# Performance work log

Measured on AMD Instinct MI355X. Metric: run time of the kernel, lower is better.

The kernel has to match this reference:

```python
import jax, jax.numpy as jnp
import numpy as np

D_MODEL = 1024
NUM_HEADS = 16
BATCH = 2
SEQ = 2048


def setup_inputs() -> dict:
    key = jax.random.key(0)
    ks = jax.random.split(key, 5)
    scale = 1.0 / np.sqrt(D_MODEL)
    x = jax.random.normal(ks[0], (BATCH, SEQ, D_MODEL), dtype=jnp.float32)
    Wq = jax.random.normal(ks[1], (D_MODEL, D_MODEL), dtype=jnp.float32) * scale
    Wk = jax.random.normal(ks[2], (D_MODEL, D_MODEL), dtype=jnp.float32) * scale
    Wv = jax.random.normal(ks[3], (D_MODEL, D_MODEL), dtype=jnp.float32) * scale
    Wo = jax.random.normal(ks[4], (D_MODEL, D_MODEL), dtype=jnp.float32) * scale
    return {"x": x, "Wq": Wq, "Wk": Wk, "Wv": Wv, "Wo": Wo}


def reference(x, Wq, Wk, Wv, Wo):
    b, s, d_model = x.shape
    h = NUM_HEADS
    d_head = d_model // h
    # projections (Linear with weight [out,in]: y = x @ W^T)
    def split_heads(y):
        return y.reshape(b, s, h, d_head).transpose(0, 2, 1, 3)  # b h s d
    q = split_heads(x @ Wq.T)
    k = split_heads(x @ Wk.T)
    v = split_heads(x @ Wv.T)
    # full (non-flash) attention, as in the original
    att = jnp.einsum('bhsd,bhtd->bhst', q, k) / jnp.sqrt(jnp.float32(d_head)).astype(x.dtype)
    att = jax.nn.softmax(att, axis=-1)
    out = jnp.einsum('bhst,bhtd->bhsd', att, v)
    out = out.transpose(0, 2, 1, 3).reshape(b, s, d_model)
    return out @ Wo.T
```

## Files before the change

### kernel.cpp

```cpp
#include <hip/hip_runtime.h>
#include <stdint.h>

typedef __bf16 bf16_t;
typedef __bf16 bf16x4 __attribute__((ext_vector_type(4)));
typedef __bf16 bf16x8 __attribute__((ext_vector_type(8)));
typedef float  f32x4  __attribute__((ext_vector_type(4)));

#define D_MODEL 1024
#define SEQ     2048
#define BATCH   2
#define NHEAD   16
#define DHEAD   64
#define NROWS   (BATCH*SEQ)
#define LDK     40
#define LDT     68

__device__ __forceinline__ int sig64(int i) { return ((i & 3) << 4) | (i >> 2); }

__device__ __forceinline__ bf16x8 cvt8(f32x4 lo, f32x4 hi) {
    bf16x8 o;
#pragma unroll
    for (int i = 0; i < 4; ++i) { o[i] = (bf16_t)lo[i]; o[4 + i] = (bf16_t)hi[i]; }
    return o;
}

__global__ void __launch_bounds__(256)
k_cvt_w(const float* __restrict__ w0, const float* __restrict__ w1,
        const float* __restrict__ w2, const float* __restrict__ w3,
        bf16_t* __restrict__ o0, bf16_t* __restrict__ o1,
        bf16_t* __restrict__ o2, bf16_t* __restrict__ o3)
{
    const int sel = blockIdx.y;
    const float*  s = (sel == 0) ? w0 : (sel == 1) ? w1 : (sel == 2) ? w2 : w3;
    bf16_t*       d = (sel == 0) ? o0 : (sel == 1) ? o1 : (sel == 2) ? o2 : o3;
    const size_t i = ((size_t)blockIdx.x * 256 + threadIdx.x) * 8;
    *(bf16x8*)(d + i) = cvt8(*(const f32x4*)(s + i), *(const f32x4*)(s + i + 4));
}

template <bool A_F32, int OUT_MODE>
__device__ __forceinline__ void gemm128(bf16_t* __restrict__ smem,
                                        const void* __restrict__ Xv,
                                        const bf16_t* __restrict__ W,
                                        void* __restrict__ Yv,
                                        int m0, int n0, float oscale)
{
    bf16_t* lA = smem;
    bf16_t* lB = smem + 128 * LDK;

    const int tid  = threadIdx.x;
    const int lane = tid & 63;
    const int w    = tid >> 6;
    const int l15  = lane & 15;
    const int quad = lane >> 4;

    const int c0 = tid, c1 = tid + 256;
    const int r0 = c0 >> 2, ks0 = c0 & 3;
    const int r1 = c1 >> 2, ks1 = c1 & 3;
    const int sO0 = r0 * LDK + ks0 * 8, sO1 = r1 * LDK + ks1 * 8;

    const bf16_t* gB0 = W + (size_t)(n0 + r0) * D_MODEL + ks0 * 8;
    const bf16_t* gB1 = W + (size_t)(n0 + r1) * D_MODEL + ks1 * 8;
    const float*  gAf0 = (const float*)Xv  + (size_t)(m0 + r0) * D_MODEL + ks0 * 8;
    const float*  gAf1 = (const float*)Xv  + (size_t)(m0 + r1) * D_MODEL + ks1 * 8;
    const bf16_t* gAh0 = (const bf16_t*)Xv + (size_t)(m0 + r0) * D_MODEL + ks0 * 8;
    const bf16_t* gAh1 = (const bf16_t*)Xv + (size_t)(m0 + r1) * D_MODEL + ks1 * 8;

    int am[4], bn[4];
    const int mw = (w >> 1) * 64, nw = (w & 1) * 64;
#pragma unroll
    for (int i = 0; i < 4; ++i) {
        am[i] = (mw + i * 16 + l15) * LDK + quad * 8;
        bn[i] = (nw + i * 16 + l15) * LDK + quad * 8;
    }

    f32x4 acc[4][4];
#pragma unroll
    for (int i = 0; i < 4; ++i)
#pragma unroll
        for (int j = 0; j < 4; ++j) acc[i][j] = f32x4{0.f, 0.f, 0.f, 0.f};

    for (int k0 = 0; k0 < D_MODEL; k0 += 32) {
        bf16x8 a0, a1;
        if constexpr (A_F32) {
            const float* p0 = gAf0 + k0;
            const float* p1 = gAf1 + k0;
            a0 = cvt8(*(const f32x4*)p0, *(const f32x4*)(p0 + 4));
            a1 = cvt8(*(const f32x4*)p1, *(const f32x4*)(p1 + 4));
        } else {
            a0 = *(const bf16x8*)(gAh0 + k0);
            a1 = *(const bf16x8*)(gAh1 + k0);
        }
        bf16x8 b0 = *(const bf16x8*)(gB0 + k0);
        bf16x8 b1 = *(const bf16x8*)(gB1 + k0);

        __syncthreads();
        *(bf16x8*)&lA[sO0] = a0;
        *(bf16x8*)&lA[sO1] = a1;
        *(bf16x8*)&lB[sO0] = b0;
        *(bf16x8*)&lB[sO1] = b1;
        __syncthreads();

        bf16x8 af[4], bfr[4];
#pragma unroll
        for (int i = 0; i < 4; ++i) af[i]  = *(const bf16x8*)&lA[am[i]];
#pragma unroll
        for (int i = 0; i < 4; ++i) bfr[i] = *(const bf16x8*)&lB[bn[i]];
#pragma unroll
        for (int mi = 0; mi < 4; ++mi)
#pragma unroll
            for (int ni = 0; ni < 4; ++ni)
                acc[mi][ni] = __builtin_amdgcn_mfma_f32_16x16x32_bf16(
                    af[mi], bfr[ni], acc[mi][ni], 0, 0, 0);
    }

    if constexpr (OUT_MODE == 1) {
        bf16_t* lT = smem;
#pragma unroll
        for (int h0 = 0; h0 < 2; ++h0) {
            __syncthreads();
            if ((w >> 1) == h0) {
#pragma unroll
                for (int mi = 0; mi < 4; ++mi)
#pragma unroll
                    for (int ni = 0; ni < 4; ++ni) {
                        bf16x4 pk;
#pragma unroll
                        for (int r = 0; r < 4; ++r)
                            pk[r] = (bf16_t)(acc[mi][ni][r] * oscale);
                        const int col = nw + ni * 16 + l15;
                        *(bf16x4*)&lT[col * LDT + mi * 16 + quad * 4] = pk;
                    }
            }
            __syncthreads();
            const int col = tid & 127;
            const int seg = tid >> 7;
            const int brow = m0 + h0 * 64;
            const int b = brow >> 11, sb = brow & 2047;
            const int cg = n0 + col;
            bf16_t* dst = (bf16_t*)Yv +
                ((size_t)((b << 4) | (cg >> 6)) * 64 + (cg & 63)) * SEQ + sb;
#pragma unroll
            for (int u = 0; u < 4; ++u) {
                bf16x8 vv;
#pragma unroll
                for (int e = 0; e < 8; ++e)
                    vv[e] = lT[col * LDT + sig64(seg * 32 + u * 8 + e)];
                *(bf16x8*)(dst + seg * 32 + u * 8) = vv;
            }
        }
    } else {
#pragma unroll
        for (int mi = 0; mi < 4; ++mi)
#pragma unroll
            for (int ni = 0; ni < 4; ++ni)
#pragma unroll
                for (int r = 0; r < 4; ++r) {
                    const int row = m0 + mw + mi * 16 + quad * 4 + r;
                    const int col = n0 + nw + ni * 16 + l15;
                    const float vv = acc[mi][ni][r] * oscale;
                    if constexpr (OUT_MODE == 0)
                        ((bf16_t*)Yv)[(size_t)row * D_MODEL + col] = (bf16_t)vv;
                    else
                        ((float*)Yv)[(size_t)row * D_MODEL + col] = vv;
                }
    }
}

__global__ void __launch_bounds__(256)
k_gemm_qkv(const float* __restrict__ X,
           const bf16_t* __restrict__ Wq, const bf16_t* __restrict__ Wk,
           const bf16_t* __restrict__ Wv,
           bf16_t* __restrict__ Qb, bf16_t* __restrict__ Kb, bf16_t* __restrict__ Vt)
{
    __shared__ __align__(16) bf16_t smem[128 * LDK * 2];
    const int sel = blockIdx.y >> 3;
    const int n0  = (blockIdx.y & 7) * 128;
    const int m0  = blockIdx.x * 128;
    if (sel == 0)      gemm128<true, 0>(smem, X, Wq, Qb, m0, n0, 0.125f);
    else if (sel == 1) gemm128<true, 0>(smem, X, Wk, Kb, m0, n0, 1.0f);
    else               gemm128<true, 1>(smem, X, Wv, Vt, m0, n0, 1.0f);
}

__global__ void __launch_bounds__(256)
k_gemm_out(const bf16_t* __restrict__ X, const bf16_t* __restrict__ W,
           float* __restrict__ Y)
{
    __shared__ __align__(16) bf16_t smem[128 * LDK * 2];
    gemm128<false, 2>(smem, X, W, Y, blockIdx.x * 128, blockIdx.y * 128, 1.0f);
}

__global__ void __launch_bounds__(256)
k_attn(const bf16_t* __restrict__ Qb, const bf16_t* __restrict__ Kb,
       const bf16_t* __restrict__ Vt, bf16_t* __restrict__ Ob)
{
    __shared__ __align__(16) bf16_t lK[64 * 72];
    __shared__ __align__(16) bf16_t lV[64 * 72];
    __shared__ __align__(16) bf16_t Pl[4][16 * 72];

    const int tid  = threadIdx.x;
    const int lane = tid & 63;
    const int w    = tid >> 6;
    const int l15  = lane & 15;
    const int quad = lane >> 4;

    const int bh = blockIdx.x;
    const int b  = bh >> 4, h = bh & 15;
    const int q0 = blockIdx.y * 64;

    const size_t base = (size_t)b * SEQ * D_MODEL + (size_t)h * DHEAD;
    const bf16_t* Qp = Qb + base;
    const bf16_t* Kp = Kb + base;
    const bf16_t* Vp = Vt + (size_t)bh * DHEAD * SEQ;

    const int qrow = q0 + w * 16 + l15;
    const bf16x8 qf0 = *(const bf16x8*)&Qp[(size_t)qrow * D_MODEL + quad * 8];
    const bf16x8 qf1 = *(const bf16x8*)&Qp[(size_t)qrow * D_MODEL + 32 + quad * 8];

    const int c0 = tid, c1 = tid + 256;
    const int r0 = c0 >> 3, ch0 = c0 & 7;
    const int r1 = c1 >> 3, ch1 = c1 & 7;
    const bf16_t* gK0 = Kp + (size_t)r0 * D_MODEL + ch0 * 8;
    const bf16_t* gK1 = Kp + (size_t)r1 * D_MODEL + ch1 * 8;
    const bf16_t* gV0 = Vp + (size_t)r0 * SEQ + ch0 * 8;
    const bf16_t* gV1 = Vp + (size_t)r1 * SEQ + ch1 * 8;
    const int sK0 = r0 * 72 + ch0 * 8, sK1 = r1 * 72 + ch1 * 8;

    bf16x8 ones;
#pragma unroll
    for (int i = 0; i < 8; ++i) ones[i] = (bf16_t)1.0f;

    f32x4 acc_o[4];
#pragma unroll
    for (int dt = 0; dt < 4; ++dt) acc_o[dt] = f32x4{0.f, 0.f, 0.f, 0.f};
    f32x4 acc_l = f32x4{0.f, 0.f, 0.f, 0.f};

    bf16_t* myP = Pl[w];

    bf16x8 pk0 = *(const bf16x8*)gK0;
    bf16x8 pk1 = *(const bf16x8*)gK1;
    bf16x8 pv0 = *(const bf16x8*)gV0;
    bf16x8 pv1 = *(const bf16x8*)gV1;

    for (int kv0 = 0; kv0 < SEQ; kv0 += 64) {
        __syncthreads();
        *(bf16x8*)&lK[sK0] = pk0;
        *(bf16x8*)&lK[sK1] = pk1;
        *(bf16x8*)&lV[sK0] = pv0;
        *(bf16x8*)&lV[sK1] = pv1;
        __syncthreads();

        const int nkv = kv0 + 64;
        if (nkv < SEQ) {
            pk0 = *(const bf16x8*)(gK0 + (size_t)nkv * D_MODEL);
            pk1 = *(const bf16x8*)(gK1 + (size_t)nkv * D_MODEL);
            pv0 = *(const bf16x8*)(gV0 + nkv);
            pv1 = *(const bf16x8*)(gV1 + nkv);
        }

        f32x4 accs[4];
#pragma unroll
        for (int jt = 0; jt < 4; ++jt) accs[jt] = f32x4{0.f, 0.f, 0.f, 0.f};
#pragma unroll
        for (int jt = 0; jt < 4; ++jt) {
            bf16x8 kf0 = *(const bf16x8*)&lK[(jt * 16 + l15) * 72 + quad * 8];
            bf16x8 kf1 = *(const bf16x8*)&lK[(jt * 16 + l15) * 72 + 32 + quad * 8];
            accs[jt] = __builtin_amdgcn_mfma_f32_16x16x32_bf16(qf0, kf0, accs[jt], 0, 0, 0);
            accs[jt] = __builtin_amdgcn_mfma_f32_16x16x32_bf16(qf1, kf1, accs[jt], 0, 0, 0);
        }

#pragma unroll
        for (int r = 0; r < 4; ++r) {
            bf16x4 pp;
#pragma unroll
            for (int jt = 0; jt < 4; ++jt) pp[jt] = (bf16_t)__expf(accs[jt][r]);
            *(bf16x4*)&myP[(quad * 4 + r) * 72 + l15 * 4] = pp;
        }

        const bf16x8 pf0 = *(const bf16x8*)&myP[l15 * 72 + quad * 8];
        const bf16x8 pf1 = *(const bf16x8*)&myP[l15 * 72 + 32 + quad * 8];

        acc_l = __builtin_amdgcn_mfma_f32_16x16x32_bf16(pf0, ones, acc_l, 0, 0, 0);
        acc_l = __builtin_amdgcn_mfma_f32_16x16x32_bf16(pf1, ones, acc_l, 0, 0, 0);

#pragma unroll
        for (int dt = 0; dt < 4; ++dt) {
            bf16x8 v0 = *(const bf16x8*)&lV[(dt * 16 + l15) * 72 + quad * 8];
            bf16x8 v1 = *(const bf16x8*)&lV[(dt * 16 + l15) * 72 + 32 + quad * 8];
            acc_o[dt] = __builtin_amdgcn_mfma_f32_16x16x32_bf16(pf0, v0, acc_o[dt], 0, 0, 0);
            acc_o[dt] = __builtin_amdgcn_mfma_f32_16x16x32_bf16(pf1, v1, acc_o[dt], 0, 0, 0);
        }
    }

#pragma unroll
    for (int dt = 0; dt < 4; ++dt)
#pragma unroll
        for (int r = 0; r < 4; ++r) {
            const int row = b * SEQ + q0 + w * 16 + quad * 4 + r;
            const int col = h * DHEAD + dt * 16 + l15;
            Ob[(size_t)row * D_MODEL + col] = (bf16_t)(acc_o[dt][r] / acc_l[r]);
        }
}

extern "C" void kernel_launch(void* const* d_in, const int* in_sizes, int n_in,
                              void* d_out, int out_size, void* d_ws, size_t ws_size,
                              hipStream_t stream)
{
    const float* x  = (const float*)d_in[0];
    const float* Wq = (const float*)d_in[1];
    const float* Wk = (const float*)d_in[2];
    const float* Wv = (const float*)d_in[3];
    const float* Wo = (const float*)d_in[4];
    float* out = (float*)d_out;

    const size_t wmat = (size_t)D_MODEL * D_MODEL;
    const size_t mat  = (size_t)NROWS * D_MODEL;
    bf16_t* Wqb = (bf16_t*)d_ws;
    bf16_t* Wkb = Wqb + wmat;
    bf16_t* Wvb = Wkb + wmat;
    bf16_t* Wob = Wvb + wmat;
    bf16_t* Qb  = Wob + wmat;
    bf16_t* Kb  = Qb + mat;
    bf16_t* Vt  = Kb + mat;
    bf16_t* Ab  = Qb;

    dim3 blk(256);
    k_cvt_w<<<dim3(512, 4), blk, 0, stream>>>(Wq, Wk, Wv, Wo, Wqb, Wkb, Wvb, Wob);
    k_gemm_qkv<<<dim3(32, 24), blk, 0, stream>>>(x, Wqb, Wkb, Wvb, Qb, Kb, Vt);
    k_attn<<<dim3(32, 32), blk, 0, stream>>>(Qb, Kb, Vt, Ab);
    k_gemm_out<<<dim3(32, 8), blk, 0, stream>>>(Ab, Wob, out);
}
```

Baseline: 203.4 us.

## Switch attention to 32x32 MFMA tiles and pre-convert x to bf16

Attention now uses 32x32x16 bf16 MFMA, with waves split across a 2x2 grid of query and key/value halves. They share a single 64x64 P tile in LDS, which adds a block barrier per kv step. The Vt layout becomes natural order, so the transposed store no longer needs the permutation. Activations x are converted to bf16 once in the conversion kernel instead of inside every QKV GEMM tile, at the cost of an extra workspace buffer and one extra pass over x.

```diff
diff --git a/kernel.cpp b/kernel.cpp
--- a/kernel.cpp
+++ b/kernel.cpp
@@ -5,6 +5,7 @@
 typedef __bf16 bf16x4 __attribute__((ext_vector_type(4)));
 typedef __bf16 bf16x8 __attribute__((ext_vector_type(8)));
 typedef float  f32x4  __attribute__((ext_vector_type(4)));
+typedef float  f32x16 __attribute__((ext_vector_type(16)));
 
 #define D_MODEL 1024
 #define SEQ     2048
@@ -13,9 +14,8 @@
 #define DHEAD   64
 #define NROWS   (BATCH*SEQ)
 #define LDK     40
-#define LDT     68
-
-__device__ __forceinline__ int sig64(int i) { return ((i & 3) << 4) | (i >> 2); }
+#define LDT     72
+#define LDA     72
 
 __device__ __forceinline__ bf16x8 cvt8(f32x4 lo, f32x4 hi) {
     bf16x8 o;
@@ -25,21 +25,28 @@
 }
 
 __global__ void __launch_bounds__(256)
-k_cvt_w(const float* __restrict__ w0, const float* __restrict__ w1,
-        const float* __restrict__ w2, const float* __restrict__ w3,
-        bf16_t* __restrict__ o0, bf16_t* __restrict__ o1,
-        bf16_t* __restrict__ o2, bf16_t* __restrict__ o3)
-{
-    const int sel = blockIdx.y;
-    const float*  s = (sel == 0) ? w0 : (sel == 1) ? w1 : (sel == 2) ? w2 : w3;
-    bf16_t*       d = (sel == 0) ? o0 : (sel == 1) ? o1 : (sel == 2) ? o2 : o3;
-    const size_t i = ((size_t)blockIdx.x * 256 + threadIdx.x) * 8;
+k_cvt(const float* __restrict__ w0, const float* __restrict__ w1,
+      const float* __restrict__ w2, const float* __restrict__ w3,
+      const float* __restrict__ x,
+      bf16_t* __restrict__ o0, bf16_t* __restrict__ o1,
+      bf16_t* __restrict__ o2, bf16_t* __restrict__ o3,
+      bf16_t* __restrict__ ox)
+{
+    const int blk = blockIdx.x;
+    const float* s; bf16_t* d; int bi;
+    if (blk < 2048) { s = x; d = ox; bi = blk; }
+    else {
+        const int t = blk - 2048, sel = t >> 9; bi = t & 511;
+        s = (sel == 0) ? w0 : (sel == 1) ? w1 : (sel == 2) ? w2 : w3;
+        d = (sel == 0) ? o0 : (sel == 1) ? o1 : (sel == 2) ? o2 : o3;
+    }
+    const size_t i = ((size_t)bi * 256 + threadIdx.x) * 8;
     *(bf16x8*)(d + i) = cvt8(*(const f32x4*)(s + i), *(const f32x4*)(s + i + 4));
 }
 
-template <bool A_F32, int OUT_MODE>
+template <int OUT_MODE>
 __device__ __forceinline__ void gemm128(bf16_t* __restrict__ smem,
-                                        const void* __restrict__ Xv,
+                                        const bf16_t* __restrict__ X,
                                         const bf16_t* __restrict__ W,
                                         void* __restrict__ Yv,
                                         int m0, int n0, float oscale)
@@ -58,12 +65,10 @@
     const int r1 = c1 >> 2, ks1 = c1 & 3;
     const int sO0 = r0 * LDK + ks0 * 8, sO1 = r1 * LDK + ks1 * 8;
 
+    const bf16_t* gA0 = X + (size_t)(m0 + r0) * D_MODEL + ks0 * 8;
+    const bf16_t* gA1 = X + (size_t)(m0 + r1) * D_MODEL + ks1 * 8;
     const bf16_t* gB0 = W + (size_t)(n0 + r0) * D_MODEL + ks0 * 8;
     const bf16_t* gB1 = W + (size_t)(n0 + r1) * D_MODEL + ks1 * 8;
-    const float*  gAf0 = (const float*)Xv  + (size_t)(m0 + r0) * D_MODEL + ks0 * 8;
-    const float*  gAf1 = (const float*)Xv  + (size_t)(m0 + r1) * D_MODEL + ks1 * 8;
-    const bf16_t* gAh0 = (const bf16_t*)Xv + (size_t)(m0 + r0) * D_MODEL + ks0 * 8;
-    const bf16_t* gAh1 = (const bf16_t*)Xv + (size_t)(m0 + r1) * D_MODEL + ks1 * 8;
 
     int am[4], bn[4];
     const int mw = (w >> 1) * 64, nw = (w & 1) * 64;
@@ -80,16 +85,8 @@
         for (int j = 0; j < 4; ++j) acc[i][j] = f32x4{0.f, 0.f, 0.f, 0.f};
 
     for (int k0 = 0; k0 < D_MODEL; k0 += 32) {
-        bf16x8 a0, a1;
-        if constexpr (A_F32) {
-            const float* p0 = gAf0 + k0;
-            const float* p1 = gAf1 + k0;
-            a0 = cvt8(*(const f32x4*)p0, *(const f32x4*)(p0 + 4));
-            a1 = cvt8(*(const f32x4*)p1, *(const f32x4*)(p1 + 4));
-        } else {
-            a0 = *(const bf16x8*)(gAh0 + k0);
-            a1 = *(const bf16x8*)(gAh1 + k0);
-        }
+        bf16x8 a0 = *(const bf16x8*)(gA0 + k0);
+        bf16x8 a1 = *(const bf16x8*)(gA1 + k0);
         bf16x8 b0 = *(const bf16x8*)(gB0 + k0);
         bf16x8 b1 = *(const bf16x8*)(gB1 + k0);
 
@@ -140,13 +137,9 @@
             bf16_t* dst = (bf16_t*)Yv +
                 ((size_t)((b << 4) | (cg >> 6)) * 64 + (cg & 63)) * SEQ + sb;
 #pragma unroll
-            for (int u = 0; u < 4; ++u) {
-                bf16x8 vv;
-#pragma unroll
-                for (int e = 0; e < 8; ++e)
-                    vv[e] = lT[col * LDT + sig64(seg * 32 + u * 8 + e)];
-                *(bf16x8*)(dst + seg * 32 + u * 8) = vv;
-            }
+            for (int u = 0; u < 4; ++u)
+                *(bf16x8*)(dst + seg * 32 + u * 8) =
+                    *(const bf16x8*)&lT[col * LDT + seg * 32 + u * 8];
         }
     } else {
 #pragma unroll
@@ -167,7 +160,7 @@
 }
 
 __global__ void __launch_bounds__(256)
-k_gemm_qkv(const float* __restrict__ X,
+k_gemm_qkv(const bf16_t* __restrict__ X,
            const bf16_t* __restrict__ Wq, const bf16_t* __restrict__ Wk,
            const bf16_t* __restrict__ Wv,
            bf16_t* __restrict__ Qb, bf16_t* __restrict__ Kb, bf16_t* __restrict__ Vt)
@@ -176,9 +169,9 @@
     const int sel = blockIdx.y >> 3;
     const int n0  = (blockIdx.y & 7) * 128;
     const int m0  = blockIdx.x * 128;
-    if (sel == 0)      gemm128<true, 0>(smem, X, Wq, Qb, m0, n0, 0.125f);
-    else if (sel == 1) gemm128<true, 0>(smem, X, Wk, Kb, m0, n0, 1.0f);
-    else               gemm128<true, 1>(smem, X, Wv, Vt, m0, n0, 1.0f);
+    if (sel == 0)      gemm128<0>(smem, X, Wq, Qb, m0, n0, 0.125f);
+    else if (sel == 1) gemm128<0>(smem, X, Wk, Kb, m0, n0, 1.0f);
+    else               gemm128<1>(smem, X, Wv, Vt, m0, n0, 1.0f);
 }
 
 __global__ void __launch_bounds__(256)
@@ -186,35 +179,39 @@
            float* __restrict__ Y)
 {
     __shared__ __align__(16) bf16_t smem[128 * LDK * 2];
-    gemm128<false, 2>(smem, X, W, Y, blockIdx.x * 128, blockIdx.y * 128, 1.0f);
-}
-
-__global__ void __launch_bounds__(256)
+    gemm128<2>(smem, X, W, Y, blockIdx.x * 128, blockIdx.y * 128, 1.0f);
+}
+
+__global__ void __launch_bounds__(256, 4)
 k_attn(const bf16_t* __restrict__ Qb, const bf16_t* __restrict__ Kb,
        const bf16_t* __restrict__ Vt, bf16_t* __restrict__ Ob)
 {
-    __shared__ __align__(16) bf16_t lK[64 * 72];
-    __shared__ __align__(16) bf16_t lV[64 * 72];
-    __shared__ __align__(16) bf16_t Pl[4][16 * 72];
+    __shared__ __align__(16) bf16_t lK[64 * LDA];
+    __shared__ __align__(16) bf16_t lV[64 * LDA];
+    __shared__ __align__(16) bf16_t Pm[64 * LDA];
 
     const int tid  = threadIdx.x;
     const int lane = tid & 63;
     const int w    = tid >> 6;
-    const int l15  = lane & 15;
-    const int quad = lane >> 4;
+    const int l31  = lane & 31;
+    const int h    = lane >> 5;
+    const int a    = w & 1;
+    const int b    = w >> 1;
 
     const int bh = blockIdx.x;
-    const int b  = bh >> 4, h = bh & 15;
+    const int b_ = bh >> 4, hh = bh & 15;
     const int q0 = blockIdx.y * 64;
 
-    const size_t base = (size_t)b * SEQ * D_MODEL + (size_t)h * DHEAD;
+    const size_t base = (size_t)b_ * SEQ * D_MODEL + (size_t)hh * DHEAD;
     const bf16_t* Qp = Qb + base;
     const bf16_t* Kp = Kb + base;
     const bf16_t* Vp = Vt + (size_t)bh * DHEAD * SEQ;
 
-    const int qrow = q0 + w * 16 + l15;
-    const bf16x8 qf0 = *(const bf16x8*)&Qp[(size_t)qrow * D_MODEL + quad * 8];
-    const bf16x8 qf1 = *(const bf16x8*)&Qp[(size_t)qrow * D_MODEL + 32 + quad * 8];
+    const int qrow = q0 + b * 32 + l31;
+    bf16x8 qf[4];
+#pragma unroll
+    for (int c = 0; c < 4; ++c)
+        qf[c] = *(const bf16x8*)&Qp[(size_t)qrow * D_MODEL + c * 16 + h * 8];
 
     const int c0 = tid, c1 = tid + 256;
     const int r0 = c0 >> 3, ch0 = c0 & 7;
@@ -223,18 +220,15 @@
     const bf16_t* gK1 = Kp + (size_t)r1 * D_MODEL + ch1 * 8;
     const bf16_t* gV0 = Vp + (size_t)r0 * SEQ + ch0 * 8;
     const bf16_t* gV1 = Vp + (size_t)r1 * SEQ + ch1 * 8;
-    const int sK0 = r0 * 72 + ch0 * 8, sK1 = r1 * 72 + ch1 * 8;
+    const int sK0 = r0 * LDA + ch0 * 8, sK1 = r1 * LDA + ch1 * 8;
 
     bf16x8 ones;
 #pragma unroll
     for (int i = 0; i < 8; ++i) ones[i] = (bf16_t)1.0f;
 
-    f32x4 acc_o[4];
-#pragma unroll
-    for (int dt = 0; dt < 4; ++dt) acc_o[dt] = f32x4{0.f, 0.f, 0.f, 0.f};
-    f32x4 acc_l = f32x4{0.f, 0.f, 0.f, 0.f};
-
-    bf16_t* myP = Pl[w];
+    f32x16 acc_o, acc_l;
+#pragma unroll
+    for (int i = 0; i < 16; ++i) { acc_o[i] = 0.f; acc_l[i] = 0.f; }
 
     bf16x8 pk0 = *(const bf16x8*)gK0;
     bf16x8 pk1 = *(const bf16x8*)gK1;
@@ -257,47 +251,42 @@
             pv1 = *(const bf16x8*)(gV1 + nkv);
         }
 
-        f32x4 accs[4];
-#pragma unroll
-        for (int jt = 0; jt < 4; ++jt) accs[jt] = f32x4{0.f, 0.f, 0.f, 0.f};
-#pragma unroll
-        for (int jt = 0; jt < 4; ++jt) {
-            bf16x8 kf0 = *(const bf16x8*)&lK[(jt * 16 + l15) * 72 + quad * 8];
-            bf16x8 kf1 = *(const bf16x8*)&lK[(jt * 16 + l15) * 72 + 32 + quad * 8];
-            accs[jt] = __builtin_amdgcn_mfma_f32_16x16x32_bf16(qf0, kf0, accs[jt], 0, 0, 0);
-            accs[jt] = __builtin_amdgcn_mfma_f32_16x16x32_bf16(qf1, kf1, accs[jt], 0, 0, 0);
-        }
-
+        f32x16 st;
+#pragma unroll
+        for (int i = 0; i < 16; ++i) st[i] = 0.f;
+#pragma unroll
+        for (int c = 0; c < 4; ++c) {
+            bf16x8 kf = *(const bf16x8*)&lK[(a * 32 + l31) * LDA + c * 16 + h * 8];
+            st = __builtin_amdgcn_mfma_f32_32x32x16_bf16(kf, qf[c], st, 0, 0, 0);
+        }
+
+#pragma unroll
+        for (int g = 0; g < 4; ++g) {
+            bf16x4 pp;
+#pragma unroll
+            for (int r = 0; r < 4; ++r) pp[r] = (bf16_t)__expf(st[g * 4 + r]);
+            *(bf16x4*)&Pm[(b * 32 + l31) * LDA + a * 32 + g * 8 + h * 4] = pp;
+        }
+        __syncthreads();
+
+#pragma unroll
+        for (int c = 0; c < 4; ++c) {
+            bf16x8 pf = *(const bf16x8*)&Pm[(b * 32 + l31) * LDA + c * 16 + h * 8];
+            bf16x8 vf = *(const bf16x8*)&lV[(a * 32 + l31) * LDA + c * 16 + h * 8];
+            acc_l = __builtin_amdgcn_mfma_f32_32x32x16_bf16(pf, ones, acc_l, 0, 0, 0);
+            acc_o = __builtin_amdgcn_mfma_f32_32x32x16_bf16(pf, vf, acc_o, 0, 0, 0);
+        }
+    }
+
+#pragma unroll
+    for (int g = 0; g < 4; ++g)
 #pragma unroll
         for (int r = 0; r < 4; ++r) {
-            bf16x4 pp;
-#pragma unroll
-            for (int jt = 0; jt < 4; ++jt) pp[jt] = (bf16_t)__expf(accs[jt][r]);
-            *(bf16x4*)&myP[(quad * 4 + r) * 72 + l15 * 4] = pp;
-        }
-
-        const bf16x8 pf0 = *(const bf16x8*)&myP[l15 * 72 + quad * 8];
-        const bf16x8 pf1 = *(const bf16x8*)&myP[l15 * 72 + 32 + quad * 8];
-
-        acc_l = __builtin_amdgcn_mfma_f32_16x16x32_bf16(pf0, ones, acc_l, 0, 0, 0);
-        acc_l = __builtin_amdgcn_mfma_f32_16x16x32_bf16(pf1, ones, acc_l, 0, 0, 0);
-
-#pragma unroll
-        for (int dt = 0; dt < 4; ++dt) {
-            bf16x8 v0 = *(const bf16x8*)&lV[(dt * 16 + l15) * 72 + quad * 8];
-            bf16x8 v1 = *(const bf16x8*)&lV[(dt * 16 + l15) * 72 + 32 + quad * 8];
-            acc_o[dt] = __builtin_amdgcn_mfma_f32_16x16x32_bf16(pf0, v0, acc_o[dt], 0, 0, 0);
-            acc_o[dt] = __builtin_amdgcn_mfma_f32_16x16x32_bf16(pf1, v1, acc_o[dt], 0, 0, 0);
-        }
-    }
-
-#pragma unroll
-    for (int dt = 0; dt < 4; ++dt)
-#pragma unroll
-        for (int r = 0; r < 4; ++r) {
-            const int row = b * SEQ + q0 + w * 16 + quad * 4 + r;
-            const int col = h * DHEAD + dt * 16 + l15;
-            Ob[(size_t)row * D_MODEL + col] = (bf16_t)(acc_o[dt][r] / acc_l[r]);
+            const int ql  = r + 8 * g + 4 * h;
+            const int row = b_ * SEQ + q0 + b * 32 + ql;
+            const int col = hh * DHEAD + a * 32 + l31;
+            Ob[(size_t)row * D_MODEL + col] =
+                (bf16_t)(acc_o[g * 4 + r] / acc_l[g * 4 + r]);
         }
 }
 
@@ -318,14 +307,15 @@
     bf16_t* Wkb = Wqb + wmat;
     bf16_t* Wvb = Wkb + wmat;
     bf16_t* Wob = Wvb + wmat;
-    bf16_t* Qb  = Wob + wmat;
+    bf16_t* Xb  = Wob + wmat;
+    bf16_t* Qb  = Xb + mat;
     bf16_t* Kb  = Qb + mat;
     bf16_t* Vt  = Kb + mat;
     bf16_t* Ab  = Qb;
 
     dim3 blk(256);
-    k_cvt_w<<<dim3(512, 4), blk, 0, stream>>>(Wq, Wk, Wv, Wo, Wqb, Wkb, Wvb, Wob);
-    k_gemm_qkv<<<dim3(32, 24), blk, 0, stream>>>(x, Wqb, Wkb, Wvb, Qb, Kb, Vt);
+    k_cvt<<<dim3(4096), blk, 0, stream>>>(Wq, Wk, Wv, Wo, x, Wqb, Wkb, Wvb, Wob, Xb);
+    k_gemm_qkv<<<dim3(32, 24), blk, 0, stream>>>(Xb, Wqb, Wkb, Wvb, Qb, Kb, Vt);
     k_attn<<<dim3(32, 32), blk, 0, stream>>>(Qb, Kb, Vt, Ab);
     k_gemm_out<<<dim3(32, 8), blk, 0, stream>>>(Ab, Wob, out);
 }
```

Measured after the change: 201.3 us. About the same (-1.0%).
